# Kernel optimization log

Measured on AMD Instinct MI355X. Metric: run time of the kernel, lower is better.

## Reference

```python
import jax, jax.numpy as jnp
import numpy as np

B, N, E, ENT, D, H, L = 64, 2048, 32768, 100000, 256, 256, 512


def setup_inputs() -> dict:
    key = jax.random.key(0)
    ks = jax.random.split(key, 12)
    return {
        "neighbors": jax.random.randint(ks[0], (B, N), 0, ENT),
        "adj_row": jax.random.randint(ks[1], (B, E), 0, N),
        "adj_col": jax.random.randint(ks[2], (B, E), 0, N),
        "adj_val": jax.random.uniform(ks[3], (B, E), dtype=jnp.float32),
        "emb_table": jax.random.normal(ks[4], (ENT, D), dtype=jnp.float32),
        "W1": jax.random.normal(ks[5], (D, H), dtype=jnp.float32) * (1.0 / np.sqrt(H)),
        "b1": jax.random.normal(ks[6], (H,), dtype=jnp.float32) * 0.01,
        "W2": jax.random.normal(ks[7], (H, H), dtype=jnp.float32) * (1.0 / np.sqrt(H)),
        "b2": jax.random.normal(ks[8], (H,), dtype=jnp.float32) * 0.01,
        "fc1_w": jax.random.normal(ks[9], (H, H), dtype=jnp.float32) * (1.0 / np.sqrt(H)),
        "fc1_b": jax.random.normal(ks[10], (H,), dtype=jnp.float32) * 0.01,
        "cur_len": L,
    }


def _gcn_layer(x, W, b, adj_row, adj_col, adj_val):
    # x: [B,N,din] -> support: [B,N,dout]
    support = jnp.einsum("bnd,dh->bnh", x, W)
    # sparse adj @ support: gather columns, scale by edge value, scatter-add to rows
    gathered = jnp.take_along_axis(support, adj_col[:, :, None], axis=1)  # [B,E,h]
    weighted = gathered * adj_val[:, :, None]
    agg = jax.vmap(lambda r, g: jax.ops.segment_sum(g, r, num_segments=N))(adj_row, weighted)
    return agg + b


def reference(neighbors, adj_row, adj_col, adj_val, emb_table, W1, b1, W2, b2, fc1_w, fc1_b, cur_len):
    x = emb_table[neighbors]                                   # [B,N,D] embedding gather
    x = _gcn_layer(x, W1, b1, adj_row, adj_col, adj_val)       # GCN layer 1
    x = _gcn_layer(x, W2, b2, adj_row, adj_col, adj_val)       # GCN layer 2
    seq = x[:, :cur_len, :]                                    # keep cur_node prefix, padded to common L
    pooled = jnp.mean(seq, axis=1, keepdims=True)              # self.seq == 'mean'
    return jax.nn.relu(jnp.einsum("blh,ho->blo", pooled, fc1_w) + fc1_b)  # [B,1,H]
```

## Files before the change

### kernel.cpp

```cpp
#include <hip/hip_runtime.h>

#define B 64
#define N 2048
#define E 32768
#define D 256
#define H 256
#define CH 32
#define SEG 8
#define EPB (E / SEG)

__global__ __launch_bounds__(512) void edge_w_kernel(
    const int* __restrict__ adj_row, const int* __restrict__ adj_col,
    const float* __restrict__ adj_val, const int* __restrict__ cur_len,
    float* __restrict__ w_out, float* __restrict__ sw_out)
{
    __shared__ float wloc[N];
    __shared__ float sred[8];
    const int b = blockIdx.x, seg = blockIdx.y, tid = threadIdx.x;
    const int L = *cur_len;

    for (int i = tid; i < N; i += 512) wloc[i] = 0.f;
    __syncthreads();

    const int base = b * E + seg * EPB;
    float svp = 0.f;
    #pragma unroll
    for (int k = 0; k < EPB / 512; ++k) {
        const int e = base + tid + k * 512;
        const int r = adj_row[e];
        if (r < L) {
            const float v = adj_val[e];
            atomicAdd(&wloc[adj_col[e]], v);
            svp += v;
        }
    }
    __syncthreads();

    #pragma unroll
    for (int i = tid; i < N; i += 512) {
        const float v = wloc[i];
        if (v != 0.f) atomicAdd(&w_out[(size_t)b * N + i], v);
    }
    for (int off = 32; off; off >>= 1) svp += __shfl_down(svp, off, 64);
    if ((tid & 63) == 0) sred[tid >> 6] = svp;
    __syncthreads();
    if (tid == 0) {
        float s = 0.f;
        #pragma unroll
        for (int i = 0; i < 8; ++i) s += sred[i];
        atomicAdd(&sw_out[b], s);
    }
}

__global__ __launch_bounds__(512) void edge_z_kernel(
    const int* __restrict__ adj_row, const int* __restrict__ adj_col,
    const float* __restrict__ adj_val, const float* __restrict__ w,
    float* __restrict__ z_out)
{
    __shared__ float zloc[N];
    const int b = blockIdx.x, seg = blockIdx.y, tid = threadIdx.x;

    for (int i = tid; i < N; i += 512) zloc[i] = 0.f;
    __syncthreads();

    const int base = b * E + seg * EPB;
    const float* __restrict__ wb = w + (size_t)b * N;
    #pragma unroll
    for (int k = 0; k < EPB / 512; ++k) {
        const int e = base + tid + k * 512;
        const float wv = wb[adj_row[e]];
        if (wv != 0.f) atomicAdd(&zloc[adj_col[e]], wv * adj_val[e]);
    }
    __syncthreads();

    #pragma unroll
    for (int i = tid; i < N; i += 512) {
        const float v = zloc[i];
        if (v != 0.f) atomicAdd(&z_out[(size_t)b * N + i], v);
    }
}

__global__ __launch_bounds__(256) void gather_kernel(
    const int* __restrict__ neighbors, const float* __restrict__ emb,
    const float* __restrict__ z, float* __restrict__ u_part)
{
    const int b = blockIdx.x, chunk = blockIdx.y, tid = threadIdx.x;
    const int lane = tid & 63, rg = tid >> 6;
    const float4* __restrict__ emb4 = (const float4*)emb;
    float4 acc0 = make_float4(0.f, 0.f, 0.f, 0.f);
    float4 acc1 = make_float4(0.f, 0.f, 0.f, 0.f);

    const int n0 = chunk * (N / CH);
    #pragma unroll 8
    for (int i = 0; i < (N / CH) / 4; ++i) {
        const int n = n0 + 4 * i + rg;
        const float zv = z[(size_t)b * N + n];
        const long idx = (long)neighbors[(size_t)b * N + n];
        const float4 v = emb4[idx * (D / 4) + lane];
        if (i & 1) {
            acc1.x += zv * v.x; acc1.y += zv * v.y;
            acc1.z += zv * v.z; acc1.w += zv * v.w;
        } else {
            acc0.x += zv * v.x; acc0.y += zv * v.y;
            acc0.z += zv * v.z; acc0.w += zv * v.w;
        }
    }
    float4 acc = make_float4(acc0.x + acc1.x, acc0.y + acc1.y,
                             acc0.z + acc1.z, acc0.w + acc1.w);

    __shared__ float4 red[256];
    red[tid] = acc;
    __syncthreads();
    if (tid < 64) {
        float4 a = red[tid], bb = red[tid + 64], c = red[tid + 128], d = red[tid + 192];
        float4 s = make_float4(a.x + bb.x + c.x + d.x, a.y + bb.y + c.y + d.y,
                               a.z + bb.z + c.z + d.z, a.w + bb.w + c.w + d.w);
        ((float4*)u_part)[((size_t)b * CH + chunk) * (D / 4) + tid] = s;
    }
}

__global__ __launch_bounds__(1024) void head_kernel(
    const float* __restrict__ u_part, const float* __restrict__ sw,
    const float* __restrict__ W1, const float* __restrict__ b1,
    const float* __restrict__ W2, const float* __restrict__ b2,
    const float* __restrict__ fc1_w, const float* __restrict__ fc1_b,
    const int* __restrict__ cur_len, float* __restrict__ out)
{
    const int b = blockIdx.x;
    const int t = threadIdx.x & 255;
    const int s = threadIdx.x >> 8;
    __shared__ float red[4][256];
    __shared__ float su[D];
    __shared__ float sy[H];
    __shared__ float sp[H];

    float part = 0.f;
    #pragma unroll
    for (int c = 0; c < 8; ++c)
        part += u_part[((size_t)b * CH + s * 8 + c) * D + t];
    red[s][t] = part;
    __syncthreads();
    if (s == 0) su[t] = red[0][t] + red[1][t] + red[2][t] + red[3][t];
    __syncthreads();

    part = 0.f;
    #pragma unroll 8
    for (int k = 0; k < 64; ++k) {
        const int d = s * 64 + k;
        part += su[d] * W1[d * H + t];
    }
    red[s][t] = part;
    __syncthreads();
    if (s == 0) sy[t] = red[0][t] + red[1][t] + red[2][t] + red[3][t] + sw[b] * b1[t];
    __syncthreads();

    const float invL = 1.f / (float)(*cur_len);
    part = 0.f;
    #pragma unroll 8
    for (int k = 0; k < 64; ++k) {
        const int d = s * 64 + k;
        part += sy[d] * W2[d * H + t];
    }
    red[s][t] = part;
    __syncthreads();
    if (s == 0)
        sp[t] = (red[0][t] + red[1][t] + red[2][t] + red[3][t]) * invL + b2[t];
    __syncthreads();

    part = 0.f;
    #pragma unroll 8
    for (int k = 0; k < 64; ++k) {
        const int d = s * 64 + k;
        part += sp[d] * fc1_w[d * H + t];
    }
    red[s][t] = part;
    __syncthreads();
    if (s == 0) {
        const float v = red[0][t] + red[1][t] + red[2][t] + red[3][t] + fc1_b[t];
        out[(size_t)b * H + t] = fmaxf(v, 0.f);
    }
}

extern "C" void kernel_launch(void* const* d_in, const int* in_sizes, int n_in,
                              void* d_out, int out_size, void* d_ws, size_t ws_size,
                              hipStream_t stream) {
    const int*   neighbors = (const int*)  d_in[0];
    const int*   adj_row   = (const int*)  d_in[1];
    const int*   adj_col   = (const int*)  d_in[2];
    const float* adj_val   = (const float*)d_in[3];
    const float* emb_table = (const float*)d_in[4];
    const float* W1        = (const float*)d_in[5];
    const float* b1        = (const float*)d_in[6];
    const float* W2        = (const float*)d_in[7];
    const float* b2        = (const float*)d_in[8];
    const float* fc1_w     = (const float*)d_in[9];
    const float* fc1_b     = (const float*)d_in[10];
    const int*   cur_len   = (const int*)  d_in[11];
    float*       out       = (float*)d_out;

    float* w_ws  = (float*)d_ws;
    float* z_ws  = w_ws + (size_t)B * N;
    float* sw_ws = z_ws + (size_t)B * N;
    float* u_ws  = sw_ws + 64;

    hipMemsetAsync(d_ws, 0, ((size_t)2 * B * N + 64) * sizeof(float), stream);

    edge_w_kernel<<<dim3(B, SEG), 512, 0, stream>>>(adj_row, adj_col, adj_val,
                                                    cur_len, w_ws, sw_ws);
    edge_z_kernel<<<dim3(B, SEG), 512, 0, stream>>>(adj_row, adj_col, adj_val,
                                                    w_ws, z_ws);
    gather_kernel<<<dim3(B, CH), 256, 0, stream>>>(neighbors, emb_table, z_ws, u_ws);
    head_kernel<<<B, 1024, 0, stream>>>(u_ws, sw_ws, W1, b1, W2, b2,
                                        fc1_w, fc1_b, cur_len, out);
}
```

Before: 231.9 us.

## Replace global atomics with per-segment partial buffers and drop memset

Each edge block now writes its full shared-memory histogram into a per-segment partial buffer instead of atomically adding into global w/z arrays. The next kernel sums the SEG partials. edge_z computes the full w vector and its sum sw into shared memory, so the w lookup becomes a shared-memory read. The gather kernel stages z and the neighbor indices in shared memory and uses four accumulators. This removes the workspace memset and the global atomic traffic, at the cost of SEG-times-larger intermediate buffers and redundant partial summation in every block.

```diff
diff --git a/kernel.cpp b/kernel.cpp
--- a/kernel.cpp
+++ b/kernel.cpp
@@ -12,10 +12,9 @@
 __global__ __launch_bounds__(512) void edge_w_kernel(
     const int* __restrict__ adj_row, const int* __restrict__ adj_col,
     const float* __restrict__ adj_val, const int* __restrict__ cur_len,
-    float* __restrict__ w_out, float* __restrict__ sw_out)
+    float* __restrict__ w_part)
 {
     __shared__ float wloc[N];
-    __shared__ float sred[8];
     const int b = blockIdx.x, seg = blockIdx.y, tid = threadIdx.x;
     const int L = *cur_len;
 
@@ -23,90 +22,103 @@
     __syncthreads();
 
     const int base = b * E + seg * EPB;
-    float svp = 0.f;
     #pragma unroll
     for (int k = 0; k < EPB / 512; ++k) {
         const int e = base + tid + k * 512;
         const int r = adj_row[e];
-        if (r < L) {
-            const float v = adj_val[e];
-            atomicAdd(&wloc[adj_col[e]], v);
-            svp += v;
-        }
-    }
-    __syncthreads();
-
-    #pragma unroll
+        if (r < L) atomicAdd(&wloc[adj_col[e]], adj_val[e]);
+    }
+    __syncthreads();
+
+    float4* dst = (float4*)(w_part + ((size_t)b * SEG + seg) * N);
+    const float4* src = (const float4*)wloc;
+    dst[tid] = src[tid];
+}
+
+__global__ __launch_bounds__(512) void edge_z_kernel(
+    const int* __restrict__ adj_row, const int* __restrict__ adj_col,
+    const float* __restrict__ adj_val, const float* __restrict__ w_part,
+    float* __restrict__ z_part, float* __restrict__ sw_out)
+{
+    __shared__ float wfull[N];
+    __shared__ float zloc[N];
+    __shared__ float sred[8];
+    const int b = blockIdx.x, seg = blockIdx.y, tid = threadIdx.x;
+
+    float swp = 0.f;
     for (int i = tid; i < N; i += 512) {
-        const float v = wloc[i];
-        if (v != 0.f) atomicAdd(&w_out[(size_t)b * N + i], v);
-    }
-    for (int off = 32; off; off >>= 1) svp += __shfl_down(svp, off, 64);
-    if ((tid & 63) == 0) sred[tid >> 6] = svp;
-    __syncthreads();
-    if (tid == 0) {
+        float s = 0.f;
+        #pragma unroll
+        for (int sg = 0; sg < SEG; ++sg)
+            s += w_part[((size_t)b * SEG + sg) * N + i];
+        wfull[i] = s;
+        zloc[i] = 0.f;
+        swp += s;
+    }
+    __syncthreads();
+
+    if (seg == 0) {
+        for (int off = 32; off; off >>= 1) swp += __shfl_down(swp, off, 64);
+        if ((tid & 63) == 0) sred[tid >> 6] = swp;
+    }
+    __syncthreads();
+    if (seg == 0 && tid == 0) {
         float s = 0.f;
         #pragma unroll
         for (int i = 0; i < 8; ++i) s += sred[i];
-        atomicAdd(&sw_out[b], s);
-    }
-}
-
-__global__ __launch_bounds__(512) void edge_z_kernel(
-    const int* __restrict__ adj_row, const int* __restrict__ adj_col,
-    const float* __restrict__ adj_val, const float* __restrict__ w,
-    float* __restrict__ z_out)
-{
-    __shared__ float zloc[N];
-    const int b = blockIdx.x, seg = blockIdx.y, tid = threadIdx.x;
-
-    for (int i = tid; i < N; i += 512) zloc[i] = 0.f;
-    __syncthreads();
+        sw_out[b] = s;
+    }
 
     const int base = b * E + seg * EPB;
-    const float* __restrict__ wb = w + (size_t)b * N;
     #pragma unroll
     for (int k = 0; k < EPB / 512; ++k) {
         const int e = base + tid + k * 512;
-        const float wv = wb[adj_row[e]];
+        const float wv = wfull[adj_row[e]];
         if (wv != 0.f) atomicAdd(&zloc[adj_col[e]], wv * adj_val[e]);
     }
     __syncthreads();
 
-    #pragma unroll
-    for (int i = tid; i < N; i += 512) {
-        const float v = zloc[i];
-        if (v != 0.f) atomicAdd(&z_out[(size_t)b * N + i], v);
-    }
+    float4* dst = (float4*)(z_part + ((size_t)b * SEG + seg) * N);
+    const float4* src = (const float4*)zloc;
+    dst[tid] = src[tid];
 }
 
 __global__ __launch_bounds__(256) void gather_kernel(
     const int* __restrict__ neighbors, const float* __restrict__ emb,
-    const float* __restrict__ z, float* __restrict__ u_part)
+    const float* __restrict__ z_part, float* __restrict__ u_part)
 {
     const int b = blockIdx.x, chunk = blockIdx.y, tid = threadIdx.x;
     const int lane = tid & 63, rg = tid >> 6;
+    const int n0 = chunk * (N / CH);
+
+    __shared__ float zs[N / CH];
+    __shared__ int   ns[N / CH];
+    if (tid < N / CH) {
+        float s = 0.f;
+        #pragma unroll
+        for (int sg = 0; sg < SEG; ++sg)
+            s += z_part[((size_t)b * SEG + sg) * N + n0 + tid];
+        zs[tid] = s;
+        ns[tid] = neighbors[(size_t)b * N + n0 + tid];
+    }
+    __syncthreads();
+
     const float4* __restrict__ emb4 = (const float4*)emb;
-    float4 acc0 = make_float4(0.f, 0.f, 0.f, 0.f);
-    float4 acc1 = make_float4(0.f, 0.f, 0.f, 0.f);
-
-    const int n0 = chunk * (N / CH);
-    #pragma unroll 8
-    for (int i = 0; i < (N / CH) / 4; ++i) {
-        const int n = n0 + 4 * i + rg;
-        const float zv = z[(size_t)b * N + n];
-        const long idx = (long)neighbors[(size_t)b * N + n];
+    float4 a0 = make_float4(0.f,0.f,0.f,0.f), a1 = a0, a2 = a0, a3 = a0;
+
+    #pragma unroll
+    for (int i = 0; i < 16; ++i) {
+        const int j = i * 4 + rg;
+        const float zv = zs[j];
+        const size_t idx = (size_t)ns[j];
         const float4 v = emb4[idx * (D / 4) + lane];
-        if (i & 1) {
-            acc1.x += zv * v.x; acc1.y += zv * v.y;
-            acc1.z += zv * v.z; acc1.w += zv * v.w;
-        } else {
-            acc0.x += zv * v.x; acc0.y += zv * v.y;
-            acc0.z += zv * v.z; acc0.w += zv * v.w;
-        }
-    }
-    float4 acc = make_float4(acc0.x + acc1.x, acc0.y + acc1.y,
-                             acc0.z + acc1.z, acc0.w + acc1.w);
+        if ((i & 3) == 0)      { a0.x += zv*v.x; a0.y += zv*v.y; a0.z += zv*v.z; a0.w += zv*v.w; }
+        else if ((i & 3) == 1) { a1.x += zv*v.x; a1.y += zv*v.y; a1.z += zv*v.z; a1.w += zv*v.w; }
+        else if ((i & 3) == 2) { a2.x += zv*v.x; a2.y += zv*v.y; a2.z += zv*v.z; a2.w += zv*v.w; }
+        else                   { a3.x += zv*v.x; a3.y += zv*v.y; a3.z += zv*v.z; a3.w += zv*v.w; }
+    }
+    float4 acc = make_float4(a0.x+a1.x+a2.x+a3.x, a0.y+a1.y+a2.y+a3.y,
+                             a0.z+a1.z+a2.z+a3.z, a0.w+a1.w+a2.w+a3.w);
 
     __shared__ float4 red[256];
     red[tid] = acc;
@@ -198,18 +210,16 @@
     const int*   cur_len   = (const int*)  d_in[11];
     float*       out       = (float*)d_out;
 
-    float* w_ws  = (float*)d_ws;
-    float* z_ws  = w_ws + (size_t)B * N;
-    float* sw_ws = z_ws + (size_t)B * N;
+    float* wp_ws = (float*)d_ws;
+    float* zp_ws = wp_ws + (size_t)B * SEG * N;
+    float* sw_ws = zp_ws + (size_t)B * SEG * N;
     float* u_ws  = sw_ws + 64;
 
-    hipMemsetAsync(d_ws, 0, ((size_t)2 * B * N + 64) * sizeof(float), stream);
-
     edge_w_kernel<<<dim3(B, SEG), 512, 0, stream>>>(adj_row, adj_col, adj_val,
-                                                    cur_len, w_ws, sw_ws);
+                                                    cur_len, wp_ws);
     edge_z_kernel<<<dim3(B, SEG), 512, 0, stream>>>(adj_row, adj_col, adj_val,
-                                                    w_ws, z_ws);
-    gather_kernel<<<dim3(B, CH), 256, 0, stream>>>(neighbors, emb_table, z_ws, u_ws);
+                                                    wp_ws, zp_ws, sw_ws);
+    gather_kernel<<<dim3(B, CH), 256, 0, stream>>>(neighbors, emb_table, zp_ws, u_ws);
     head_kernel<<<B, 1024, 0, stream>>>(u_ws, sw_ws, W1, b1, W2, b2,
                                         fc1_w, fc1_b, cur_len, out);
 }
```

Result: faster. 227.0 us (-2.1%).
